# Optimization experiments

Hardware: AMD Instinct MI355X
Metric: run time of the kernel (lower is better)

Reference implementation:

```python
import jax, jax.numpy as jnp
import numpy as np

K = 17
PAD = K // 2
THRESHOLD = 55.0
TEMPERATURE = 20.0


def _normalize_0_100(x, eps=1e-8):
    x_min = jnp.min(x)
    x_max = jnp.max(x)
    return 100.0 * (x - x_min) / jnp.maximum(x_max - x_min, eps)


def setup_inputs() -> dict:
    key = jax.random.key(0)
    k1, k2, k3, k4 = jax.random.split(key, 4)
    H_total, W_total = 512, 512
    Fdim, Odim = 100, 180
    f_print1 = jax.random.uniform(k1, (H_total, W_total), dtype=jnp.float32)
    freq_ind = jax.random.randint(k2, (H_total, W_total), 0, Fdim)
    orient_ind = jax.random.randint(k3, (H_total, W_total), 0, Odim)
    filterbank = jax.random.normal(k4, (Fdim, Odim, K, K), dtype=jnp.float32)
    return {
        "f_print1": f_print1,
        "freq_ind": freq_ind,
        "orient_ind": orient_ind,
        "filterbank": filterbank,
        "H": 480,
        "W": 480,
        "margin": 32,
    }


def reference(f_print1, freq_ind, orient_ind, filterbank, H, W, margin):
    Fdim, Odim, K1, K2 = filterbank.shape
    H_total, W_total = f_print1.shape
    # im2col: zero-padded sliding KxK windows, row-major over the kernel window
    # (matches torch F.unfold ordering for a single channel)
    x_pad = jnp.pad(f_print1, PAD)
    ih = jnp.arange(H_total)[:, None] + jnp.arange(K)[None, :]  # (H_total, K)
    iw = jnp.arange(W_total)[:, None] + jnp.arange(K)[None, :]  # (W_total, K)
    patches = x_pad[ih[:, None, :, None], iw[None, :, None, :]]  # (H,W,K,K)

    # per-pixel kernel gather (indices are 1-based in the source, clamped)
    f0 = jnp.clip(freq_ind - 1, 0, Fdim - 1)
    o0 = jnp.clip(orient_ind - 1, 0, Odim - 1)
    idx = f0 * Odim + o0  # (H,W)
    kernels = filterbank.reshape(Fdim * Odim, K, K)[idx]  # (H,W,K,K)

    # spatially-varying convolution: per-pixel multiply + reduce
    y = jnp.einsum('hwkl,hwkl->hw', patches, kernels)

    out = _normalize_0_100(y)
    out = 100.0 * jax.nn.sigmoid(TEMPERATURE * (out / 100.0 - THRESHOLD / 100.0))
    out = _normalize_0_100(out)
    return out
```

## Files before the change

### kernel.cpp

```cpp
#include <hip/hip_runtime.h>
#include <math.h>

#define FDIM  100
#define ODIM  180
#define HTOT  512
#define WTOT  512
#define TILE  32
#define REG   48
#define LDSW  49
#define NSLICE 8
#define SLICE_SZ 2250
#define NTILE 256
#define NBLK  (NTILE * NSLICE)
#define TEMPERATURE 20.0f
#define THRESHOLD   55.0f

typedef float f32x4 __attribute__((ext_vector_type(4)));

__global__ __launch_bounds__(256) void filter_sliced(
    const float* __restrict__ x,
    const int*   __restrict__ freq,
    const int*   __restrict__ orient,
    const float* __restrict__ fb,
    float*       __restrict__ y,
    float2*      __restrict__ partial)
{
    __shared__ float tile[REG][LDSW];
    __shared__ int   sel[TILE * TILE];
    __shared__ unsigned int nsel;

    const int gid   = blockIdx.x;
    const int slice = gid & (NSLICE - 1);
    const int t     = gid >> 3;
    const int bx    = t & 15, by = t >> 4;
    const int tid   = threadIdx.x;
    const int lane  = tid & 63;

    if (tid == 0) nsel = 0;
    __syncthreads();

    const int lo = slice * SLICE_SZ;
    #pragma unroll
    for (int k = 0; k < 4; ++k) {
        const int p  = tid + k * 256;
        const int pr = p >> 5, pc = p & 31;
        const int pid = (by * TILE + pr) * WTOT + bx * TILE + pc;
        int f0 = freq[pid] - 1;
        int o0 = orient[pid] - 1;
        f0 = f0 < 0 ? 0 : (f0 > FDIM - 1 ? FDIM - 1 : f0);
        o0 = o0 < 0 ? 0 : (o0 > ODIM - 1 ? ODIM - 1 : o0);
        const int idx = f0 * ODIM + o0;
        const bool want = (idx >= lo && idx < lo + SLICE_SZ);
        const unsigned long long mask = __ballot(want);
        unsigned int base = 0;
        if (lane == 0) base = atomicAdd(&nsel, (unsigned int)__popcll(mask));
        base = __shfl(base, 0, 64);
        if (want) {
            const int pos = __popcll(mask & ((1ULL << lane) - 1ULL));
            sel[base + pos] = (idx << 10) | p;
        }
    }

    const int h0 = by * TILE - 8;
    const int w0 = bx * TILE - 8;
    for (int i = tid; i < REG * REG; i += 256) {
        const int r = i / REG, c = i - r * REG;
        const int gh = h0 + r, gw = w0 + c;
        float v = 0.f;
        if (gh >= 0 && gh < HTOT && gw >= 0 && gw < WTOT)
            v = x[gh * WTOT + gw];
        tile[r][c] = v;
    }
    __syncthreads();

    const unsigned int m = nsel;
    const int l  = tid & 15;
    const int qw = tid >> 4;

    int offs[18];
    #pragma unroll
    for (int j = 0; j < 18; ++j) {
        const int e = j * 16 + l;
        offs[j] = (e / 17) * LDSW + (e % 17);
    }

    float mn = 3.4e38f, mx = -3.4e38f;

    for (unsigned int s = qw; s < m; s += 16) {
        const int packed = sel[s];
        const int tp  = packed & 1023;
        const int ppy = tp >> 5, ppx = tp & 31;
        const float* __restrict__ kf = fb + (size_t)(packed >> 10) * 289;

        float kv[18];
        #pragma unroll
        for (int j = 0; j < 18; ++j) kv[j] = kf[j * 16 + l];
        const float kt = kf[288];

        const float* __restrict__ base = &tile[ppy][ppx];
        float a0 = 0.f, a1 = 0.f, a2 = 0.f, a3 = 0.f;
        #pragma unroll
        for (int j = 0; j < 16; j += 4) {
            a0 = fmaf(kv[j    ], base[offs[j    ]], a0);
            a1 = fmaf(kv[j + 1], base[offs[j + 1]], a1);
            a2 = fmaf(kv[j + 2], base[offs[j + 2]], a2);
            a3 = fmaf(kv[j + 3], base[offs[j + 3]], a3);
        }
        a0 = fmaf(kv[16], base[offs[16]], a0);
        a1 = fmaf(kv[17], base[offs[17]], a1);
        float acc = (a0 + a1) + (a2 + a3);
        if (l == 0) acc = fmaf(kt, base[16 * LDSW + 16], acc);

        #pragma unroll
        for (int off = 8; off; off >>= 1)
            acc += __shfl_xor(acc, off, 64);

        if (l == 0)
            y[(by * TILE + ppy) * WTOT + bx * TILE + ppx] = acc;
        mn = fminf(mn, acc);
        mx = fmaxf(mx, acc);
    }

    #pragma unroll
    for (int off = 32; off > 0; off >>= 1) {
        mn = fminf(mn, __shfl_down(mn, off, 64));
        mx = fmaxf(mx, __shfl_down(mx, off, 64));
    }
    __shared__ float smn[4], smx[4];
    const int wid = tid >> 6;
    if (lane == 0) { smn[wid] = mn; smx[wid] = mx; }
    __syncthreads();
    if (tid == 0) {
        float bmn = smn[0], bmx = smx[0];
        #pragma unroll
        for (int i = 1; i < 4; ++i) {
            bmn = fminf(bmn, smn[i]);
            bmx = fmaxf(bmx, smx[i]);
        }
        partial[gid] = make_float2(bmn, bmx);
    }
}

__global__ __launch_bounds__(256) void filter_final(
    float* __restrict__ y,
    const float2* __restrict__ partial)
{
    const int tid = threadIdx.x;
    float mn = 3.4e38f, mx = -3.4e38f;
    for (int i = tid; i < NBLK; i += 256) {
        const float2 p = partial[i];
        mn = fminf(mn, p.x);
        mx = fmaxf(mx, p.y);
    }
    #pragma unroll
    for (int off = 32; off > 0; off >>= 1) {
        mn = fminf(mn, __shfl_down(mn, off, 64));
        mx = fmaxf(mx, __shfl_down(mx, off, 64));
    }
    __shared__ float smn[4], smx[4];
    const int wid = tid >> 6, lane = tid & 63;
    if (lane == 0) { smn[wid] = mn; smx[wid] = mx; }
    __syncthreads();
    __shared__ float sfin[2];
    if (tid == 0) {
        float bmn = smn[0], bmx = smx[0];
        #pragma unroll
        for (int i = 1; i < 4; ++i) {
            bmn = fminf(bmn, smn[i]);
            bmx = fmaxf(bmx, smx[i]);
        }
        sfin[0] = bmn; sfin[1] = bmx;
    }
    __syncthreads();

    const float ymin = sfin[0];
    const float rng  = fmaxf(sfin[1] - ymin, 1e-8f);
    const float smin = 100.f / (1.f + expf( 11.f));
    const float smax = 100.f / (1.f + expf(-9.f));
    const float srng = fmaxf(smax - smin, 1e-8f);

    const int base = blockIdx.x * 1024 + tid * 4;
    f32x4 v = *reinterpret_cast<const f32x4*>(&y[base]);
    #pragma unroll
    for (int i = 0; i < 4; ++i) {
        const float o1 = 100.f * (v[i] - ymin) / rng;
        const float s  = 100.f / (1.f + expf(-(TEMPERATURE * (o1 * 0.01f - THRESHOLD * 0.01f))));
        v[i] = 100.f * (s - smin) / srng;
    }
    *reinterpret_cast<f32x4*>(&y[base]) = v;
}

extern "C" void kernel_launch(void* const* d_in, const int* in_sizes, int n_in,
                              void* d_out, int out_size, void* d_ws, size_t ws_size,
                              hipStream_t stream) {
    const float* x      = (const float*)d_in[0];
    const int*   freq   = (const int*)d_in[1];
    const int*   orient = (const int*)d_in[2];
    const float* fb     = (const float*)d_in[3];
    float*       out    = (float*)d_out;
    float2*      partial = (float2*)d_ws;

    filter_sliced<<<dim3(NBLK), 256, 0, stream>>>(x, freq, orient, fb, out, partial);

    filter_final<<<(HTOT * WTOT) / 1024, 256, 0, stream>>>(out, partial);
}
```

Before: 34.13 us.

## Shrink tiles to 32x16 with 128-thread blocks and rotate kernel-row offsets

The sliced filter kernel moves from 32x32 pixel tiles with 256 threads to 32x16 tiles with 128 threads, doubling the block count and adding an occupancy hint to spread work more evenly. Alternate 16-lane groups rotate their kernel-element order by 9 rows, aiming to cut LDS bank conflicts between concurrent pixels. The final kernel reads the per-block partials as float4 and processes 2 elements per thread over twice as many blocks. Smaller tiles raise halo overhead, so each output pixel now costs more LDS fill traffic.

```diff
diff --git a/kernel.cpp b/kernel.cpp
--- a/kernel.cpp
+++ b/kernel.cpp
@@ -5,19 +5,20 @@
 #define ODIM  180
 #define HTOT  512
 #define WTOT  512
-#define TILE  32
-#define REG   48
+#define TW    32
+#define TH    16
 #define LDSW  49
 #define NSLICE 8
 #define SLICE_SZ 2250
-#define NTILE 256
+#define NTILE 512
 #define NBLK  (NTILE * NSLICE)
 #define TEMPERATURE 20.0f
 #define THRESHOLD   55.0f
 
+typedef float f32x2 __attribute__((ext_vector_type(2)));
 typedef float f32x4 __attribute__((ext_vector_type(4)));
 
-__global__ __launch_bounds__(256) void filter_sliced(
+__global__ __launch_bounds__(128, 8) void filter_sliced(
     const float* __restrict__ x,
     const int*   __restrict__ freq,
     const int*   __restrict__ orient,
@@ -25,8 +26,8 @@
     float*       __restrict__ y,
     float2*      __restrict__ partial)
 {
-    __shared__ float tile[REG][LDSW];
-    __shared__ int   sel[TILE * TILE];
+    __shared__ float tile[2 * TH][LDSW];
+    __shared__ int   sel[TW * TH];
     __shared__ unsigned int nsel;
 
     const int gid   = blockIdx.x;
@@ -42,9 +43,9 @@
     const int lo = slice * SLICE_SZ;
     #pragma unroll
     for (int k = 0; k < 4; ++k) {
-        const int p  = tid + k * 256;
+        const int p  = tid + k * 128;
         const int pr = p >> 5, pc = p & 31;
-        const int pid = (by * TILE + pr) * WTOT + bx * TILE + pc;
+        const int pid = (by * TH + pr) * WTOT + bx * TW + pc;
         int f0 = freq[pid] - 1;
         int o0 = orient[pid] - 1;
         f0 = f0 < 0 ? 0 : (f0 > FDIM - 1 ? FDIM - 1 : f0);
@@ -57,14 +58,14 @@
         base = __shfl(base, 0, 64);
         if (want) {
             const int pos = __popcll(mask & ((1ULL << lane) - 1ULL));
-            sel[base + pos] = (idx << 10) | p;
-        }
-    }
-
-    const int h0 = by * TILE - 8;
-    const int w0 = bx * TILE - 8;
-    for (int i = tid; i < REG * REG; i += 256) {
-        const int r = i / REG, c = i - r * REG;
+            sel[base + pos] = (idx << 9) | p;
+        }
+    }
+
+    const int h0 = by * TH - 8;
+    const int w0 = bx * TW - 8;
+    for (int i = tid; i < 32 * 48; i += 128) {
+        const int r = i / 48, c = i - r * 48;
         const int gh = h0 + r, gw = w0 + c;
         float v = 0.f;
         if (gh >= 0 && gh < HTOT && gw >= 0 && gw < WTOT)
@@ -77,24 +78,30 @@
     const int l  = tid & 15;
     const int qw = tid >> 4;
 
+    const int rot = (qw & 1) * 9;
+
     int offs[18];
     #pragma unroll
     for (int j = 0; j < 18; ++j) {
-        const int e = j * 16 + l;
+        int jr = j + rot; if (jr >= 18) jr -= 18;
+        const int e = jr * 16 + l;
         offs[j] = (e / 17) * LDSW + (e % 17);
     }
 
     float mn = 3.4e38f, mx = -3.4e38f;
 
-    for (unsigned int s = qw; s < m; s += 16) {
+    for (unsigned int s = qw; s < m; s += 8) {
         const int packed = sel[s];
-        const int tp  = packed & 1023;
+        const int tp  = packed & 511;
         const int ppy = tp >> 5, ppx = tp & 31;
-        const float* __restrict__ kf = fb + (size_t)(packed >> 10) * 289;
+        const float* __restrict__ kf = fb + (size_t)(packed >> 9) * 289;
 
         float kv[18];
         #pragma unroll
-        for (int j = 0; j < 18; ++j) kv[j] = kf[j * 16 + l];
+        for (int j = 0; j < 18; ++j) {
+            int jr = j + rot; if (jr >= 18) jr -= 18;
+            kv[j] = kf[jr * 16 + l];
+        }
         const float kt = kf[288];
 
         const float* __restrict__ base = &tile[ppy][ppx];
@@ -116,7 +123,7 @@
             acc += __shfl_xor(acc, off, 64);
 
         if (l == 0)
-            y[(by * TILE + ppy) * WTOT + bx * TILE + ppx] = acc;
+            y[(by * TH + ppy) * WTOT + bx * TW + ppx] = acc;
         mn = fminf(mn, acc);
         mx = fmaxf(mx, acc);
     }
@@ -126,17 +133,13 @@
         mn = fminf(mn, __shfl_down(mn, off, 64));
         mx = fmaxf(mx, __shfl_down(mx, off, 64));
     }
-    __shared__ float smn[4], smx[4];
+    __shared__ float smn[2], smx[2];
     const int wid = tid >> 6;
     if (lane == 0) { smn[wid] = mn; smx[wid] = mx; }
     __syncthreads();
     if (tid == 0) {
-        float bmn = smn[0], bmx = smx[0];
-        #pragma unroll
-        for (int i = 1; i < 4; ++i) {
-            bmn = fminf(bmn, smn[i]);
-            bmx = fmaxf(bmx, smx[i]);
-        }
+        const float bmn = fminf(smn[0], smn[1]);
+        const float bmx = fmaxf(smx[0], smx[1]);
         partial[gid] = make_float2(bmn, bmx);
     }
 }
@@ -147,10 +150,11 @@
 {
     const int tid = threadIdx.x;
     float mn = 3.4e38f, mx = -3.4e38f;
-    for (int i = tid; i < NBLK; i += 256) {
-        const float2 p = partial[i];
-        mn = fminf(mn, p.x);
-        mx = fmaxf(mx, p.y);
+    const f32x4* __restrict__ p4 = reinterpret_cast<const f32x4*>(partial);
+    for (int i = tid; i < NBLK / 2; i += 256) {
+        const f32x4 p = p4[i];
+        mn = fminf(mn, fminf(p.x, p.z));
+        mx = fmaxf(mx, fmaxf(p.y, p.w));
     }
     #pragma unroll
     for (int off = 32; off > 0; off >>= 1) {
@@ -179,15 +183,15 @@
     const float smax = 100.f / (1.f + expf(-9.f));
     const float srng = fmaxf(smax - smin, 1e-8f);
 
-    const int base = blockIdx.x * 1024 + tid * 4;
-    f32x4 v = *reinterpret_cast<const f32x4*>(&y[base]);
-    #pragma unroll
-    for (int i = 0; i < 4; ++i) {
+    const int base = blockIdx.x * 512 + tid * 2;
+    f32x2 v = *reinterpret_cast<const f32x2*>(&y[base]);
+    #pragma unroll
+    for (int i = 0; i < 2; ++i) {
         const float o1 = 100.f * (v[i] - ymin) / rng;
         const float s  = 100.f / (1.f + expf(-(TEMPERATURE * (o1 * 0.01f - THRESHOLD * 0.01f))));
         v[i] = 100.f * (s - smin) / srng;
     }
-    *reinterpret_cast<f32x4*>(&y[base]) = v;
+    *reinterpret_cast<f32x2*>(&y[base]) = v;
 }
 
 extern "C" void kernel_launch(void* const* d_in, const int* in_sizes, int n_in,
@@ -200,7 +204,7 @@
     float*       out    = (float*)d_out;
     float2*      partial = (float2*)d_ws;
 
-    filter_sliced<<<dim3(NBLK), 256, 0, stream>>>(x, freq, orient, fb, out, partial);
-
-    filter_final<<<(HTOT * WTOT) / 1024, 256, 0, stream>>>(out, partial);
+    filter_sliced<<<dim3(NBLK), 128, 0, stream>>>(x, freq, orient, fb, out, partial);
+
+    filter_final<<<(HTOT * WTOT) / 512, 256, 0, stream>>>(out, partial);
 }
```

After: 116.7 us. 242% more time.
